# Kernel optimization log

Measured on AMD Instinct MI355X. Metric: run time of the kernel, lower is better.

Reference implementation:

```python
import jax, jax.numpy as jnp
from jax import lax
import numpy as np

K_F = 3                      # propagation kernel
NUM = K_F * K_F - 1          # 8 non-reference neighbors
IDX_REF = NUM // 2           # 4
PROP_TIME = 18
GAMMA = 0.5                  # affinity_gamma (TGASS)
EPS_AFF = 1e-8


def setup_inputs() -> dict:
    key = jax.random.key(0)
    k1, k2, k3, k4, k5 = jax.random.split(key, 5)
    B, H, W = 4, 352, 1216
    feat_init = jax.random.uniform(k1, (B, 1, H, W), jnp.float32) * 10.0   # initial depth
    guidance = jax.random.normal(k2, (B, NUM, H, W), jnp.float32)
    confidence = jax.random.uniform(k3, (B, 1, H, W), jnp.float32)
    # conv_offset_aff: Conv2d(ch_g=8 -> 3*num=24, k=3, pad=1). Zero-init in the
    # module is a training init; use small random weights for a meaningful test.
    w_oa = jax.random.normal(k4, (3 * NUM, NUM, 3, 3), jnp.float32) * 0.05
    b_oa = jax.random.normal(k5, (3 * NUM,), jnp.float32) * 0.01
    aff_scale = jnp.array([GAMMA * NUM], jnp.float32)  # TGASS learnable scale
    return {"feat_init": feat_init, "guidance": guidance, "confidence": confidence,
            "w_oa": w_oa, "b_oa": b_oa, "aff_scale": aff_scale}


def _offset_affinity(guidance, w_oa, b_oa, aff_scale):
    B, _, H, W = guidance.shape
    oa = lax.conv_general_dilated(guidance, w_oa, (1, 1), "SAME",
                                  dimension_numbers=("NCHW", "OIHW", "NCHW"))
    oa = oa + b_oa[None, :, None, None]
    o1, o2, aff = jnp.split(oa, 3, axis=1)            # each [B, 8, H, W]
    offset = jnp.concatenate([o1, o2], axis=1).reshape(B, NUM, 2, H, W)
    zeros_ref = jnp.zeros((B, 1, 2, H, W), offset.dtype)
    offset = jnp.concatenate([offset[:, :IDX_REF], zeros_ref, offset[:, IDX_REF:]],
                             axis=1).reshape(B, -1, H, W)  # [B, 2*9, H, W]
    # TGASS affinity
    aff = jnp.tanh(aff) / (aff_scale[0] + EPS_AFF)
    aff_abs_sum = jnp.sum(jnp.abs(aff), axis=1, keepdims=True) + 1e-4
    aff_abs_sum = jnp.maximum(aff_abs_sum, 1.0)       # TGASS clamp to >= 1
    aff = aff / aff_abs_sum
    aff_ref = 1.0 - jnp.sum(aff, axis=1, keepdims=True)
    aff = jnp.concatenate([aff[:, :IDX_REF], aff_ref, aff[:, IDX_REF:]], axis=1)
    return offset, aff                                 # [B,18,H,W], [B,9,H,W]


def _bilinear(f, ys, xs):
    # f: [H, W]; ys, xs: [K, H, W] float sample coords. Zero outside bounds (DCNv2).
    H, W = f.shape
    y0 = jnp.floor(ys); x0 = jnp.floor(xs)
    wy1 = ys - y0; wy0 = 1.0 - wy1
    wx1 = xs - x0; wx0 = 1.0 - wx1

    def g(yi, xi):
        valid = (yi >= 0) & (yi <= H - 1) & (xi >= 0) & (xi <= W - 1)
        yc = jnp.clip(yi, 0, H - 1).astype(jnp.int32)
        xc = jnp.clip(xi, 0, W - 1).astype(jnp.int32)
        return jnp.where(valid, f[yc, xc], 0.0)

    return (wy0 * wx0 * g(y0, x0) + wy0 * wx1 * g(y0, x0 + 1)
            + wy1 * wx0 * g(y0 + 1, x0) + wy1 * wx1 * g(y0 + 1, x0 + 1))


def _dcn(feat, offset, aff):
    # Modulated deformable conv with w=ones, b=0, stride=1, pad=1, groups=1.
    # feat [B,1,H,W], offset [B,2*9,H,W] ((dy,dx) pairs), aff [B,9,H,W] modulation.
    B, _, H, W = feat.shape
    KK = K_F * K_F
    off = offset.reshape(B, KK, 2, H, W)
    k = jnp.arange(KK)
    ky = (k // K_F - 1).astype(feat.dtype)            # kernel taps, pad=1
    kx = (k % K_F - 1).astype(feat.dtype)
    yg, xg = jnp.meshgrid(jnp.arange(H, dtype=feat.dtype),
                          jnp.arange(W, dtype=feat.dtype), indexing="ij")
    ys = yg[None, None] + ky[None, :, None, None] + off[:, :, 0]  # [B,9,H,W]
    xs = xg[None, None] + kx[None, :, None, None] + off[:, :, 1]
    sampled = jax.vmap(_bilinear)(feat[:, 0], ys, xs)             # [B,9,H,W]
    return jnp.sum(aff * sampled, axis=1, keepdims=True)          # [B,1,H,W]


def reference(feat_init, guidance, confidence, w_oa, b_oa, aff_scale):
    offset, aff = _offset_affinity(guidance, w_oa, b_oa, aff_scale)

    def step(feat, _):
        feat = _dcn(feat * confidence, offset, aff)
        return feat, None

    feat, _ = lax.scan(step, feat_init, None, length=PROP_TIME)
    return feat
```

## Files before the change

kernel.cpp:

```cpp
#include <hip/hip_runtime.h>

#define BB 4
#define HH 352
#define WW 1216
#define HW (HH * WW)
#define NPIX (BB * HW)
#define TX 4
#define CONV_THREADS 320

#define PAD_T 5
#define PAD_L 8
#define HP (HH + 2 * PAD_T)
#define WP (WW + 2 * PAD_L)
#define HWP (HP * WP)

#define TROWS 13
#define TCOLS 76
#define TSIZE (TROWS * TCOLS)


__global__ __launch_bounds__(CONV_THREADS) void conv_offsets_kernel(
    const float* __restrict__ guid, const float* __restrict__ w,
    const float* __restrict__ bias, unsigned* __restrict__ coordp)
{
    int tid = threadIdx.x;
    if (tid >= WW / TX) return;
    int bid = blockIdx.x;
    int row = (bid & 7) * 176 + (bid >> 3);
    int y = row % HH;
    int b = row / HH;
    int x0 = tid * TX;
    const float* gb = guid + (size_t)b * 8 * HW;

    float acc[16][TX];
#pragma unroll
    for (int o = 0; o < 16; ++o) {
        float bv = bias[o];
#pragma unroll
        for (int tx = 0; tx < TX; ++tx) acc[o][tx] = bv;
    }

#pragma unroll 1
    for (int c = 0; c < 8; ++c) {
        float g[3][6];
#pragma unroll
        for (int r = 0; r < 3; ++r) {
            int yy = y + r - 1;
            bool rv = (yy >= 0) && (yy < HH);
            const float* gr = gb + (size_t)c * HW + (size_t)yy * WW;
            if (rv) {
                const float4 m = *(const float4*)(gr + x0);
                g[r][1] = m.x; g[r][2] = m.y; g[r][3] = m.z; g[r][4] = m.w;
                g[r][0] = (x0 > 0) ? gr[x0 - 1] : 0.f;
                g[r][5] = (x0 + TX < WW) ? gr[x0 + TX] : 0.f;
            } else {
#pragma unroll
                for (int i = 0; i < 6; ++i) g[r][i] = 0.f;
            }
        }
#pragma unroll
        for (int r = 0; r < 3; ++r) {
#pragma unroll
            for (int i = 0; i < 3; ++i) {
                int tap = r * 3 + i;
#pragma unroll
                for (int o = 0; o < 16; ++o) {
                    float wv = w[o * 72 + c * 9 + tap];
#pragma unroll
                    for (int tx = 0; tx < TX; ++tx)
                        acc[o][tx] = fmaf(wv, g[r][i + tx], acc[o][tx]);
                }
            }
        }
    }

    int idx0 = row * WW + x0;
#pragma unroll
    for (int n = 0; n < 8; ++n) {
        int k = (n < 4) ? n : n + 1;
        float ky = (float)(k / 3 - 1), kx = (float)(k % 3 - 1);
        unsigned cw[TX];
#pragma unroll
        for (int tx = 0; tx < TX; ++tx) {
            float yr = ky + acc[2 * n][tx];
            float xr = kx + acc[2 * n + 1][tx];
            int yq = (int)lrintf((yr + 4.f) * 8192.f);
            int xq = (int)lrintf((xr + 4.f) * 8192.f);
            yq = min(max(yq, 0), 65535);
            xq = min(max(xq, 0), 65535);
            cw[tx] = (unsigned)yq | ((unsigned)xq << 16);
        }
        uint4 v = make_uint4(cw[0], cw[1], cw[2], cw[3]);
        *(uint4*)(coordp + (size_t)n * NPIX + idx0) = v;
    }
}

__global__ __launch_bounds__(CONV_THREADS) void conv_aff_kernel(
    const float* __restrict__ guid, const float* __restrict__ w,
    const float* __restrict__ bias, const float* __restrict__ scale_p,
    unsigned short* __restrict__ affp)
{
    int tid = threadIdx.x;
    if (tid >= WW / TX) return;
    int bid = blockIdx.x;
    int row = (bid & 7) * 176 + (bid >> 3);
    int y = row % HH;
    int b = row / HH;
    int x0 = tid * TX;
    const float* gb = guid + (size_t)b * 8 * HW;

    float acc[8][TX];
#pragma unroll
    for (int o = 0; o < 8; ++o) {
        float bv = bias[16 + o];
#pragma unroll
        for (int tx = 0; tx < TX; ++tx) acc[o][tx] = bv;
    }

#pragma unroll 1
    for (int c = 0; c < 8; ++c) {
        float g[3][6];
#pragma unroll
        for (int r = 0; r < 3; ++r) {
            int yy = y + r - 1;
            bool rv = (yy >= 0) && (yy < HH);
            const float* gr = gb + (size_t)c * HW + (size_t)yy * WW;
            if (rv) {
                const float4 m = *(const float4*)(gr + x0);
                g[r][1] = m.x; g[r][2] = m.y; g[r][3] = m.z; g[r][4] = m.w;
                g[r][0] = (x0 > 0) ? gr[x0 - 1] : 0.f;
                g[r][5] = (x0 + TX < WW) ? gr[x0 + TX] : 0.f;
            } else {
#pragma unroll
                for (int i = 0; i < 6; ++i) g[r][i] = 0.f;
            }
        }
#pragma unroll
        for (int r = 0; r < 3; ++r) {
#pragma unroll
            for (int i = 0; i < 3; ++i) {
                int tap = r * 3 + i;
#pragma unroll
                for (int o = 0; o < 8; ++o) {
                    float wv = w[(16 + o) * 72 + c * 9 + tap];
#pragma unroll
                    for (int tx = 0; tx < TX; ++tx)
                        acc[o][tx] = fmaf(wv, g[r][i + tx], acc[o][tx]);
                }
            }
        }
    }

    float sc = scale_p[0] + 1e-8f;
    unsigned short av[9][TX];

#pragma unroll
    for (int tx = 0; tx < TX; ++tx) {
        float a[8];
        float asum = 1e-4f;
#pragma unroll
        for (int n = 0; n < 8; ++n) {
            a[n] = tanhf(acc[n][tx]) / sc;
            asum += fabsf(a[n]);
        }
        asum = fmaxf(asum, 1.0f);
        float ssum = 0.f;
#pragma unroll
        for (int n = 0; n < 8; ++n) { a[n] = a[n] / asum; ssum += a[n]; }
        float aref = 1.0f - ssum;
#pragma unroll
        for (int k = 0; k < 9; ++k) {
            float aval = (k == 4) ? aref : a[(k < 4) ? k : k - 1];
            int q = (int)lrintf((aval + 1.f) * 20000.f);
            q = min(max(q, 0), 65535);
            av[k][tx] = (unsigned short)q;
        }
    }

    int idx0 = row * WW + x0;
#pragma unroll
    for (int k = 0; k < 9; ++k) {
        ushort4 v = make_ushort4(av[k][0], av[k][1], av[k][2], av[k][3]);
        *(ushort4*)(affp + (size_t)k * NPIX + idx0) = v;
    }
}

template <bool MULCONF>
__global__ __launch_bounds__(256) void prop_step_kernel(
    const float* __restrict__ fsrc, const unsigned short* __restrict__ affp,
    const unsigned* __restrict__ coordp, const float* __restrict__ conf,
    float* __restrict__ dst)
{
    __shared__ float tile[TSIZE];

    int bid = blockIdx.x;
    int xcd = bid & 7;
    int s = bid >> 3;
    int yband = xcd * 11 + s % 11;
    int rest = s / 11;
    int xb = rest % 19;
    int b = rest / 19;
    int t = threadIdx.x;
    int lx = t & 63, ly = t >> 6;
    int x = xb * 64 + lx;
    int y = yband * 4 + ly;
    int idx = (b * HH + y) * WW + x;

    unsigned cw[8];
#pragma unroll
    for (int n = 0; n < 8; ++n) cw[n] = coordp[(size_t)n * NPIX + idx];
    float ak[9];
#pragma unroll
    for (int k = 0; k < 9; ++k)
        ak[k] = fmaf((float)affp[(size_t)k * NPIX + idx], 5e-5f, -1.f);
    float cv = MULCONF ? conf[idx] : 0.f;

    {
        const float* gsrc = fsrc + (size_t)b * HWP
                          + (size_t)(yband * 4 + 1) * WP + (xb * 64 + 4);
        for (int i = t; i < TSIZE; i += 256)
            tile[i] = gsrc[(i / TCOLS) * WP + (i % TCOLS)];
    }
    __syncthreads();

    float fy = (float)ly;
    float fx = (float)lx;
    float res = ak[4] * tile[(ly + 4) * TCOLS + (lx + 4)];
#pragma unroll
    for (int n = 0; n < 8; ++n) {
        float ys = fmaf((float)(cw[n] & 0xffffu), 1.f / 8192.f, fy);
        float xs = fmaf((float)(cw[n] >> 16),     1.f / 8192.f, fx);
        float y0f = floorf(ys), x0f = floorf(xs);
        float wy1 = ys - y0f, wx1 = xs - x0f;
        float wy0 = 1.f - wy1, wx0 = 1.f - wx1;
        int o = (int)y0f * TCOLS + (int)x0f;
        float v00 = tile[o],         v01 = tile[o + 1];
        float v10 = tile[o + TCOLS], v11 = tile[o + TCOLS + 1];
        float sv = wy0 * (wx0 * v00 + wx1 * v01) + wy1 * (wx0 * v10 + wx1 * v11);
        int k = (n < 4) ? n : n + 1;
        res = fmaf(ak[k], sv, res);
    }
    if (MULCONF) {
        res *= cv;
        dst[(size_t)b * HWP + (y + PAD_T) * WP + (x + PAD_L)] = res;
    } else {
        dst[idx] = res;
    }
}

__global__ __launch_bounds__(256) void zero_kernel(float4* __restrict__ p, int n4)
{
    int i = blockIdx.x * blockDim.x + threadIdx.x;
    if (i < n4) p[i] = make_float4(0.f, 0.f, 0.f, 0.f);
}

__global__ __launch_bounds__(256) void mulpad_kernel(
    const float* __restrict__ a, const float* __restrict__ c, float* __restrict__ o)
{
    int t = threadIdx.x;
    int x = blockIdx.x * 64 + (t & 63);
    int y = blockIdx.y * 4 + (t >> 6);
    int b = blockIdx.z;
    int idx = (b * HH + y) * WW + x;
    o[(size_t)b * HWP + (y + PAD_T) * WP + (x + PAD_L)] = a[idx] * c[idx];
}

extern "C" void kernel_launch(void* const* d_in, const int* in_sizes, int n_in,
                              void* d_out, int out_size, void* d_ws, size_t ws_size,
                              hipStream_t stream)
{
    const float* feat_init  = (const float*)d_in[0];
    const float* guidance   = (const float*)d_in[1];
    const float* confidence = (const float*)d_in[2];
    const float* w_oa       = (const float*)d_in[3];
    const float* b_oa       = (const float*)d_in[4];
    const float* aff_scale  = (const float*)d_in[5];
    float* out = (float*)d_out;

    const size_t N = (size_t)NPIX;
    unsigned short* affp = (unsigned short*)d_ws;
    unsigned* coordp = (unsigned*)(affp + 9 * N);
    float* fc0 = (float*)(coordp + 8 * N);
    float* fc1 = fc0 + (size_t)BB * HWP;

    const dim3 mgrid(WW / 64, HH / 4, BB);
    const int n4 = 2 * BB * HWP / 4;
    zero_kernel<<<(n4 + 255) / 256, 256, 0, stream>>>((float4*)fc0, n4);
    mulpad_kernel<<<mgrid, 256, 0, stream>>>(feat_init, confidence, fc0);
    conv_offsets_kernel<<<BB * HH, CONV_THREADS, 0, stream>>>(
        guidance, w_oa, b_oa, coordp);
    conv_aff_kernel<<<BB * HH, CONV_THREADS, 0, stream>>>(
        guidance, w_oa, b_oa, aff_scale, affp);

    const int pblocks = (WW / 64) * (HH / 4) * BB;
    float* bufs[2] = {fc0, fc1};
    const int T = 18;
    for (int i = 0; i < T; ++i) {
        const float* src = bufs[i & 1];
        if (i < T - 1) {
            float* dst = bufs[(i + 1) & 1];
            prop_step_kernel<true><<<pblocks, 256, 0, stream>>>(
                src, affp, coordp, confidence, dst);
        } else {
            prop_step_kernel<false><<<pblocks, 256, 0, stream>>>(
                src, affp, coordp, confidence, out);
        }
    }
}
```

Baseline: 589.1 us.

## Interleave per-pixel coords and affinities into one 64-byte record table

Replaces the planar coordinate (8 planes) and affinity (9 planes) arrays with an array-of-structs table holding 16 words per pixel, so each propagation step loads three uint4s plus one word per pixel instead of 17 strided scalar loads. The conv kernels now handle 2 pixels per thread with 640 threads and write the record layout. The record is padded to 64 bytes, so per-step traffic rises slightly (about 64 bytes against 50), in exchange for fewer, wider, contiguous load instructions.

```diff
diff --git a/kernel.cpp b/kernel.cpp
--- a/kernel.cpp
+++ b/kernel.cpp
@@ -5,8 +5,6 @@
 #define WW 1216
 #define HW (HH * WW)
 #define NPIX (BB * HW)
-#define TX 4
-#define CONV_THREADS 320
 
 #define PAD_T 5
 #define PAD_L 8
@@ -19,43 +17,46 @@
 #define TSIZE (TROWS * TCOLS)
 
 
-__global__ __launch_bounds__(CONV_THREADS) void conv_offsets_kernel(
+#define OTX 2
+#define OTHREADS 640
+
+__global__ __launch_bounds__(OTHREADS) void conv_offsets_kernel(
     const float* __restrict__ guid, const float* __restrict__ w,
-    const float* __restrict__ bias, unsigned* __restrict__ coordp)
+    const float* __restrict__ bias, unsigned* __restrict__ tab)
 {
     int tid = threadIdx.x;
-    if (tid >= WW / TX) return;
+    if (tid >= WW / OTX) return;
     int bid = blockIdx.x;
     int row = (bid & 7) * 176 + (bid >> 3);
     int y = row % HH;
     int b = row / HH;
-    int x0 = tid * TX;
+    int x0 = tid * OTX;
     const float* gb = guid + (size_t)b * 8 * HW;
 
-    float acc[16][TX];
+    float acc[16][OTX];
 #pragma unroll
     for (int o = 0; o < 16; ++o) {
         float bv = bias[o];
 #pragma unroll
-        for (int tx = 0; tx < TX; ++tx) acc[o][tx] = bv;
+        for (int tx = 0; tx < OTX; ++tx) acc[o][tx] = bv;
     }
 
 #pragma unroll 1
     for (int c = 0; c < 8; ++c) {
-        float g[3][6];
+        float g[3][4];
 #pragma unroll
         for (int r = 0; r < 3; ++r) {
             int yy = y + r - 1;
             bool rv = (yy >= 0) && (yy < HH);
             const float* gr = gb + (size_t)c * HW + (size_t)yy * WW;
             if (rv) {
-                const float4 m = *(const float4*)(gr + x0);
-                g[r][1] = m.x; g[r][2] = m.y; g[r][3] = m.z; g[r][4] = m.w;
+                const float2 m = *(const float2*)(gr + x0);
+                g[r][1] = m.x; g[r][2] = m.y;
                 g[r][0] = (x0 > 0) ? gr[x0 - 1] : 0.f;
-                g[r][5] = (x0 + TX < WW) ? gr[x0 + TX] : 0.f;
+                g[r][3] = (x0 + OTX < WW) ? gr[x0 + OTX] : 0.f;
             } else {
 #pragma unroll
-                for (int i = 0; i < 6; ++i) g[r][i] = 0.f;
+                for (int i = 0; i < 4; ++i) g[r][i] = 0.f;
             }
         }
 #pragma unroll
@@ -67,7 +68,7 @@
                 for (int o = 0; o < 16; ++o) {
                     float wv = w[o * 72 + c * 9 + tap];
 #pragma unroll
-                    for (int tx = 0; tx < TX; ++tx)
+                    for (int tx = 0; tx < OTX; ++tx)
                         acc[o][tx] = fmaf(wv, g[r][i + tx], acc[o][tx]);
                 }
             }
@@ -76,63 +77,64 @@
 
     int idx0 = row * WW + x0;
 #pragma unroll
-    for (int n = 0; n < 8; ++n) {
-        int k = (n < 4) ? n : n + 1;
-        float ky = (float)(k / 3 - 1), kx = (float)(k % 3 - 1);
-        unsigned cw[TX];
-#pragma unroll
-        for (int tx = 0; tx < TX; ++tx) {
+    for (int tx = 0; tx < OTX; ++tx) {
+        unsigned cw[8];
+#pragma unroll
+        for (int n = 0; n < 8; ++n) {
+            int k = (n < 4) ? n : n + 1;
+            float ky = (float)(k / 3 - 1), kx = (float)(k % 3 - 1);
             float yr = ky + acc[2 * n][tx];
             float xr = kx + acc[2 * n + 1][tx];
             int yq = (int)lrintf((yr + 4.f) * 8192.f);
             int xq = (int)lrintf((xr + 4.f) * 8192.f);
             yq = min(max(yq, 0), 65535);
             xq = min(max(xq, 0), 65535);
-            cw[tx] = (unsigned)yq | ((unsigned)xq << 16);
-        }
-        uint4 v = make_uint4(cw[0], cw[1], cw[2], cw[3]);
-        *(uint4*)(coordp + (size_t)n * NPIX + idx0) = v;
-    }
-}
-
-__global__ __launch_bounds__(CONV_THREADS) void conv_aff_kernel(
+            cw[n] = (unsigned)yq | ((unsigned)xq << 16);
+        }
+        unsigned* rec = tab + (size_t)(idx0 + tx) * 16;
+        *(uint4*)(rec)     = make_uint4(cw[0], cw[1], cw[2], cw[3]);
+        *(uint4*)(rec + 4) = make_uint4(cw[4], cw[5], cw[6], cw[7]);
+    }
+}
+
+__global__ __launch_bounds__(OTHREADS) void conv_aff_kernel(
     const float* __restrict__ guid, const float* __restrict__ w,
     const float* __restrict__ bias, const float* __restrict__ scale_p,
-    unsigned short* __restrict__ affp)
+    unsigned* __restrict__ tab)
 {
     int tid = threadIdx.x;
-    if (tid >= WW / TX) return;
+    if (tid >= WW / OTX) return;
     int bid = blockIdx.x;
     int row = (bid & 7) * 176 + (bid >> 3);
     int y = row % HH;
     int b = row / HH;
-    int x0 = tid * TX;
+    int x0 = tid * OTX;
     const float* gb = guid + (size_t)b * 8 * HW;
 
-    float acc[8][TX];
+    float acc[8][OTX];
 #pragma unroll
     for (int o = 0; o < 8; ++o) {
         float bv = bias[16 + o];
 #pragma unroll
-        for (int tx = 0; tx < TX; ++tx) acc[o][tx] = bv;
+        for (int tx = 0; tx < OTX; ++tx) acc[o][tx] = bv;
     }
 
 #pragma unroll 1
     for (int c = 0; c < 8; ++c) {
-        float g[3][6];
+        float g[3][4];
 #pragma unroll
         for (int r = 0; r < 3; ++r) {
             int yy = y + r - 1;
             bool rv = (yy >= 0) && (yy < HH);
             const float* gr = gb + (size_t)c * HW + (size_t)yy * WW;
             if (rv) {
-                const float4 m = *(const float4*)(gr + x0);
-                g[r][1] = m.x; g[r][2] = m.y; g[r][3] = m.z; g[r][4] = m.w;
+                const float2 m = *(const float2*)(gr + x0);
+                g[r][1] = m.x; g[r][2] = m.y;
                 g[r][0] = (x0 > 0) ? gr[x0 - 1] : 0.f;
-                g[r][5] = (x0 + TX < WW) ? gr[x0 + TX] : 0.f;
+                g[r][3] = (x0 + OTX < WW) ? gr[x0 + OTX] : 0.f;
             } else {
 #pragma unroll
-                for (int i = 0; i < 6; ++i) g[r][i] = 0.f;
+                for (int i = 0; i < 4; ++i) g[r][i] = 0.f;
             }
         }
 #pragma unroll
@@ -144,7 +146,7 @@
                 for (int o = 0; o < 8; ++o) {
                     float wv = w[(16 + o) * 72 + c * 9 + tap];
 #pragma unroll
-                    for (int tx = 0; tx < TX; ++tx)
+                    for (int tx = 0; tx < OTX; ++tx)
                         acc[o][tx] = fmaf(wv, g[r][i + tx], acc[o][tx]);
                 }
             }
@@ -152,10 +154,10 @@
     }
 
     float sc = scale_p[0] + 1e-8f;
-    unsigned short av[9][TX];
-
-#pragma unroll
-    for (int tx = 0; tx < TX; ++tx) {
+    int idx0 = row * WW + x0;
+
+#pragma unroll
+    for (int tx = 0; tx < OTX; ++tx) {
         float a[8];
         float asum = 1e-4f;
 #pragma unroll
@@ -168,28 +170,27 @@
 #pragma unroll
         for (int n = 0; n < 8; ++n) { a[n] = a[n] / asum; ssum += a[n]; }
         float aref = 1.0f - ssum;
+
+        unsigned av[9];
 #pragma unroll
         for (int k = 0; k < 9; ++k) {
             float aval = (k == 4) ? aref : a[(k < 4) ? k : k - 1];
             int q = (int)lrintf((aval + 1.f) * 20000.f);
-            q = min(max(q, 0), 65535);
-            av[k][tx] = (unsigned short)q;
-        }
-    }
-
-    int idx0 = row * WW + x0;
-#pragma unroll
-    for (int k = 0; k < 9; ++k) {
-        ushort4 v = make_ushort4(av[k][0], av[k][1], av[k][2], av[k][3]);
-        *(ushort4*)(affp + (size_t)k * NPIX + idx0) = v;
+            av[k] = (unsigned)min(max(q, 0), 65535);
+        }
+        unsigned* rec = tab + (size_t)(idx0 + tx) * 16;
+        *(uint4*)(rec + 8) = make_uint4(av[0] | (av[1] << 16),
+                                        av[2] | (av[3] << 16),
+                                        av[4] | (av[5] << 16),
+                                        av[6] | (av[7] << 16));
+        rec[12] = av[8];
     }
 }
 
 template <bool MULCONF>
 __global__ __launch_bounds__(256) void prop_step_kernel(
-    const float* __restrict__ fsrc, const unsigned short* __restrict__ affp,
-    const unsigned* __restrict__ coordp, const float* __restrict__ conf,
-    float* __restrict__ dst)
+    const float* __restrict__ fsrc, const unsigned* __restrict__ tab,
+    const float* __restrict__ conf, float* __restrict__ dst)
 {
     __shared__ float tile[TSIZE];
 
@@ -206,13 +207,11 @@
     int y = yband * 4 + ly;
     int idx = (b * HH + y) * WW + x;
 
-    unsigned cw[8];
-#pragma unroll
-    for (int n = 0; n < 8; ++n) cw[n] = coordp[(size_t)n * NPIX + idx];
-    float ak[9];
-#pragma unroll
-    for (int k = 0; k < 9; ++k)
-        ak[k] = fmaf((float)affp[(size_t)k * NPIX + idx], 5e-5f, -1.f);
+    const uint4* rp = (const uint4*)(tab + (size_t)idx * 16);
+    uint4 c0 = rp[0];
+    uint4 c1 = rp[1];
+    uint4 au = rp[2];
+    unsigned a8 = tab[(size_t)idx * 16 + 12];
     float cv = MULCONF ? conf[idx] : 0.f;
 
     {
@@ -223,13 +222,22 @@
     }
     __syncthreads();
 
+    unsigned cwv[8] = {c0.x, c0.y, c0.z, c0.w, c1.x, c1.y, c1.z, c1.w};
+    unsigned akU[9] = {au.x & 0xffffu, au.x >> 16, au.y & 0xffffu, au.y >> 16,
+                       au.z & 0xffffu, au.z >> 16, au.w & 0xffffu, au.w >> 16,
+                       a8 & 0xffffu};
+
     float fy = (float)ly;
     float fx = (float)lx;
-    float res = ak[4] * tile[(ly + 4) * TCOLS + (lx + 4)];
+    float a4 = fmaf((float)akU[4], 5e-5f, -1.f);
+    float res = a4 * tile[(ly + 4) * TCOLS + (lx + 4)];
 #pragma unroll
     for (int n = 0; n < 8; ++n) {
-        float ys = fmaf((float)(cw[n] & 0xffffu), 1.f / 8192.f, fy);
-        float xs = fmaf((float)(cw[n] >> 16),     1.f / 8192.f, fx);
+        int k = (n < 4) ? n : n + 1;
+        float ak = fmaf((float)akU[k], 5e-5f, -1.f);
+        unsigned q = cwv[n];
+        float ys = fmaf((float)(q & 0xffffu), 1.f / 8192.f, fy);
+        float xs = fmaf((float)(q >> 16),     1.f / 8192.f, fx);
         float y0f = floorf(ys), x0f = floorf(xs);
         float wy1 = ys - y0f, wx1 = xs - x0f;
         float wy0 = 1.f - wy1, wx0 = 1.f - wx1;
@@ -237,8 +245,7 @@
         float v00 = tile[o],         v01 = tile[o + 1];
         float v10 = tile[o + TCOLS], v11 = tile[o + TCOLS + 1];
         float sv = wy0 * (wx0 * v00 + wx1 * v01) + wy1 * (wx0 * v10 + wx1 * v11);
-        int k = (n < 4) ? n : n + 1;
-        res = fmaf(ak[k], sv, res);
+        res = fmaf(ak, sv, res);
     }
     if (MULCONF) {
         res *= cv;
@@ -278,19 +285,18 @@
     float* out = (float*)d_out;
 
     const size_t N = (size_t)NPIX;
-    unsigned short* affp = (unsigned short*)d_ws;
-    unsigned* coordp = (unsigned*)(affp + 9 * N);
-    float* fc0 = (float*)(coordp + 8 * N);
+    unsigned* tab = (unsigned*)d_ws;
+    float* fc0 = (float*)(tab + 16 * N);
     float* fc1 = fc0 + (size_t)BB * HWP;
 
     const dim3 mgrid(WW / 64, HH / 4, BB);
     const int n4 = 2 * BB * HWP / 4;
     zero_kernel<<<(n4 + 255) / 256, 256, 0, stream>>>((float4*)fc0, n4);
     mulpad_kernel<<<mgrid, 256, 0, stream>>>(feat_init, confidence, fc0);
-    conv_offsets_kernel<<<BB * HH, CONV_THREADS, 0, stream>>>(
-        guidance, w_oa, b_oa, coordp);
-    conv_aff_kernel<<<BB * HH, CONV_THREADS, 0, stream>>>(
-        guidance, w_oa, b_oa, aff_scale, affp);
+    conv_offsets_kernel<<<BB * HH, OTHREADS, 0, stream>>>(
+        guidance, w_oa, b_oa, tab);
+    conv_aff_kernel<<<BB * HH, OTHREADS, 0, stream>>>(
+        guidance, w_oa, b_oa, aff_scale, tab);
 
     const int pblocks = (WW / 64) * (HH / 4) * BB;
     float* bufs[2] = {fc0, fc1};
@@ -300,10 +306,10 @@
         if (i < T - 1) {
             float* dst = bufs[(i + 1) & 1];
             prop_step_kernel<true><<<pblocks, 256, 0, stream>>>(
-                src, affp, coordp, confidence, dst);
+                src, tab, confidence, dst);
         } else {
             prop_step_kernel<false><<<pblocks, 256, 0, stream>>>(
-                src, affp, coordp, confidence, out);
-        }
-    }
-}
+                src, tab, confidence, out);
+        }
+    }
+}
```

Result: slower. 649.1 us (+10.2%).

## Fuse offset and affinity convolutions into one shared-memory tiled kernel

Applied to the files above, without the earlier changes.

Replaces the two separate row-based convolution kernels (offsets and affinity) with a single kernel that computes all 24 output channels per pixel. Guidance data for a 64x4 tile plus halo is staged in shared memory, so each input is read once instead of twice from global memory and neighbouring rows are reused. Each thread now handles one pixel instead of four, which gives up register reuse of weights across pixels and narrows stores to scalar writes. The convolution is a small part of the total time next to the 18 propagation steps.

```diff
diff --git a/kernel.cpp b/kernel.cpp
--- a/kernel.cpp
+++ b/kernel.cpp
@@ -5,8 +5,6 @@
 #define WW 1216
 #define HW (HH * WW)
 #define NPIX (BB * HW)
-#define TX 4
-#define CONV_THREADS 320
 
 #define PAD_T 5
 #define PAD_L 8
@@ -18,170 +16,92 @@
 #define TCOLS 76
 #define TSIZE (TROWS * TCOLS)
 
-
-__global__ __launch_bounds__(CONV_THREADS) void conv_offsets_kernel(
+#define GT_W 66
+#define GT_CH 396
+#define GT_SIZE (8 * GT_CH)
+
+
+__global__ __launch_bounds__(256) void conv_fused_kernel(
     const float* __restrict__ guid, const float* __restrict__ w,
-    const float* __restrict__ bias, unsigned* __restrict__ coordp)
-{
-    int tid = threadIdx.x;
-    if (tid >= WW / TX) return;
-    int bid = blockIdx.x;
-    int row = (bid & 7) * 176 + (bid >> 3);
-    int y = row % HH;
-    int b = row / HH;
-    int x0 = tid * TX;
-    const float* gb = guid + (size_t)b * 8 * HW;
-
-    float acc[16][TX];
-#pragma unroll
-    for (int o = 0; o < 16; ++o) {
-        float bv = bias[o];
-#pragma unroll
-        for (int tx = 0; tx < TX; ++tx) acc[o][tx] = bv;
-    }
+    const float* __restrict__ bias, const float* __restrict__ scale_p,
+    unsigned short* __restrict__ affp, unsigned* __restrict__ coordp)
+{
+    __shared__ float gt[GT_SIZE];
+
+    int bx = blockIdx.x, by = blockIdx.y, b = blockIdx.z;
+    int t = threadIdx.x;
+    int lx = t & 63, ly = t >> 6;
+    int x = bx * 64 + lx;
+    int y = by * 4 + ly;
+
+    {
+        const float* gb = guid + (size_t)b * 8 * HW;
+        int gy0 = by * 4 - 1, gx0 = bx * 64 - 1;
+        for (int i = t; i < GT_SIZE; i += 256) {
+            int c = i / GT_CH, rem = i - c * GT_CH;
+            int r = rem / GT_W, col = rem - r * GT_W;
+            int gy = gy0 + r, gx = gx0 + col;
+            float v = 0.f;
+            if (gy >= 0 && gy < HH && gx >= 0 && gx < WW)
+                v = gb[(size_t)c * HW + gy * WW + gx];
+            gt[i] = v;
+        }
+    }
+    __syncthreads();
+
+    float acc[24];
+#pragma unroll
+    for (int o = 0; o < 24; ++o) acc[o] = bias[o];
 
 #pragma unroll 1
     for (int c = 0; c < 8; ++c) {
-        float g[3][6];
-#pragma unroll
-        for (int r = 0; r < 3; ++r) {
-            int yy = y + r - 1;
-            bool rv = (yy >= 0) && (yy < HH);
-            const float* gr = gb + (size_t)c * HW + (size_t)yy * WW;
-            if (rv) {
-                const float4 m = *(const float4*)(gr + x0);
-                g[r][1] = m.x; g[r][2] = m.y; g[r][3] = m.z; g[r][4] = m.w;
-                g[r][0] = (x0 > 0) ? gr[x0 - 1] : 0.f;
-                g[r][5] = (x0 + TX < WW) ? gr[x0 + TX] : 0.f;
-            } else {
-#pragma unroll
-                for (int i = 0; i < 6; ++i) g[r][i] = 0.f;
-            }
+        float v[9];
+#pragma unroll
+        for (int r = 0; r < 3; ++r)
+#pragma unroll
+            for (int i = 0; i < 3; ++i)
+                v[r * 3 + i] = gt[c * GT_CH + (ly + r) * GT_W + lx + i];
+#pragma unroll
+        for (int tap = 0; tap < 9; ++tap) {
+#pragma unroll
+            for (int o = 0; o < 24; ++o)
+                acc[o] = fmaf(w[o * 72 + c * 9 + tap], v[tap], acc[o]);
         }
-#pragma unroll
-        for (int r = 0; r < 3; ++r) {
-#pragma unroll
-            for (int i = 0; i < 3; ++i) {
-                int tap = r * 3 + i;
-#pragma unroll
-                for (int o = 0; o < 16; ++o) {
-                    float wv = w[o * 72 + c * 9 + tap];
-#pragma unroll
-                    for (int tx = 0; tx < TX; ++tx)
-                        acc[o][tx] = fmaf(wv, g[r][i + tx], acc[o][tx]);
-                }
-            }
-        }
-    }
-
-    int idx0 = row * WW + x0;
+    }
+
+    float sc = scale_p[0] + 1e-8f;
+    float a[8];
+    float asum = 1e-4f;
+#pragma unroll
+    for (int n = 0; n < 8; ++n) {
+        a[n] = tanhf(acc[16 + n]) / sc;
+        asum += fabsf(a[n]);
+    }
+    asum = fmaxf(asum, 1.0f);
+    float ssum = 0.f;
+#pragma unroll
+    for (int n = 0; n < 8; ++n) { a[n] = a[n] / asum; ssum += a[n]; }
+    float aref = 1.0f - ssum;
+
+    int idx = (b * HH + y) * WW + x;
 #pragma unroll
     for (int n = 0; n < 8; ++n) {
         int k = (n < 4) ? n : n + 1;
         float ky = (float)(k / 3 - 1), kx = (float)(k % 3 - 1);
-        unsigned cw[TX];
-#pragma unroll
-        for (int tx = 0; tx < TX; ++tx) {
-            float yr = ky + acc[2 * n][tx];
-            float xr = kx + acc[2 * n + 1][tx];
-            int yq = (int)lrintf((yr + 4.f) * 8192.f);
-            int xq = (int)lrintf((xr + 4.f) * 8192.f);
-            yq = min(max(yq, 0), 65535);
-            xq = min(max(xq, 0), 65535);
-            cw[tx] = (unsigned)yq | ((unsigned)xq << 16);
-        }
-        uint4 v = make_uint4(cw[0], cw[1], cw[2], cw[3]);
-        *(uint4*)(coordp + (size_t)n * NPIX + idx0) = v;
-    }
-}
-
-__global__ __launch_bounds__(CONV_THREADS) void conv_aff_kernel(
-    const float* __restrict__ guid, const float* __restrict__ w,
-    const float* __restrict__ bias, const float* __restrict__ scale_p,
-    unsigned short* __restrict__ affp)
-{
-    int tid = threadIdx.x;
-    if (tid >= WW / TX) return;
-    int bid = blockIdx.x;
-    int row = (bid & 7) * 176 + (bid >> 3);
-    int y = row % HH;
-    int b = row / HH;
-    int x0 = tid * TX;
-    const float* gb = guid + (size_t)b * 8 * HW;
-
-    float acc[8][TX];
-#pragma unroll
-    for (int o = 0; o < 8; ++o) {
-        float bv = bias[16 + o];
-#pragma unroll
-        for (int tx = 0; tx < TX; ++tx) acc[o][tx] = bv;
-    }
-
-#pragma unroll 1
-    for (int c = 0; c < 8; ++c) {
-        float g[3][6];
-#pragma unroll
-        for (int r = 0; r < 3; ++r) {
-            int yy = y + r - 1;
-            bool rv = (yy >= 0) && (yy < HH);
-            const float* gr = gb + (size_t)c * HW + (size_t)yy * WW;
-            if (rv) {
-                const float4 m = *(const float4*)(gr + x0);
-                g[r][1] = m.x; g[r][2] = m.y; g[r][3] = m.z; g[r][4] = m.w;
-                g[r][0] = (x0 > 0) ? gr[x0 - 1] : 0.f;
-                g[r][5] = (x0 + TX < WW) ? gr[x0 + TX] : 0.f;
-            } else {
-#pragma unroll
-                for (int i = 0; i < 6; ++i) g[r][i] = 0.f;
-            }
-        }
-#pragma unroll
-        for (int r = 0; r < 3; ++r) {
-#pragma unroll
-            for (int i = 0; i < 3; ++i) {
-                int tap = r * 3 + i;
-#pragma unroll
-                for (int o = 0; o < 8; ++o) {
-                    float wv = w[(16 + o) * 72 + c * 9 + tap];
-#pragma unroll
-                    for (int tx = 0; tx < TX; ++tx)
-                        acc[o][tx] = fmaf(wv, g[r][i + tx], acc[o][tx]);
-                }
-            }
-        }
-    }
-
-    float sc = scale_p[0] + 1e-8f;
-    unsigned short av[9][TX];
-
-#pragma unroll
-    for (int tx = 0; tx < TX; ++tx) {
-        float a[8];
-        float asum = 1e-4f;
-#pragma unroll
-        for (int n = 0; n < 8; ++n) {
-            a[n] = tanhf(acc[n][tx]) / sc;
-            asum += fabsf(a[n]);
-        }
-        asum = fmaxf(asum, 1.0f);
-        float ssum = 0.f;
-#pragma unroll
-        for (int n = 0; n < 8; ++n) { a[n] = a[n] / asum; ssum += a[n]; }
-        float aref = 1.0f - ssum;
-#pragma unroll
-        for (int k = 0; k < 9; ++k) {
-            float aval = (k == 4) ? aref : a[(k < 4) ? k : k - 1];
-            int q = (int)lrintf((aval + 1.f) * 20000.f);
-            q = min(max(q, 0), 65535);
-            av[k][tx] = (unsigned short)q;
-        }
-    }
-
-    int idx0 = row * WW + x0;
+        float yr = ky + acc[2 * n];
+        float xr = kx + acc[2 * n + 1];
+        int yq = (int)lrintf((yr + 4.f) * 8192.f);
+        int xq = (int)lrintf((xr + 4.f) * 8192.f);
+        yq = min(max(yq, 0), 65535);
+        xq = min(max(xq, 0), 65535);
+        coordp[(size_t)n * NPIX + idx] = (unsigned)yq | ((unsigned)xq << 16);
+    }
 #pragma unroll
     for (int k = 0; k < 9; ++k) {
-        ushort4 v = make_ushort4(av[k][0], av[k][1], av[k][2], av[k][3]);
-        *(ushort4*)(affp + (size_t)k * NPIX + idx0) = v;
+        float aval = (k == 4) ? aref : a[(k < 4) ? k : k - 1];
+        int q = (int)lrintf((aval + 1.f) * 20000.f);
+        q = min(max(q, 0), 65535);
+        affp[(size_t)k * NPIX + idx] = (unsigned short)q;
     }
 }
 
@@ -287,10 +207,8 @@
     const int n4 = 2 * BB * HWP / 4;
     zero_kernel<<<(n4 + 255) / 256, 256, 0, stream>>>((float4*)fc0, n4);
     mulpad_kernel<<<mgrid, 256, 0, stream>>>(feat_init, confidence, fc0);
-    conv_offsets_kernel<<<BB * HH, CONV_THREADS, 0, stream>>>(
-        guidance, w_oa, b_oa, coordp);
-    conv_aff_kernel<<<BB * HH, CONV_THREADS, 0, stream>>>(
-        guidance, w_oa, b_oa, aff_scale, affp);
+    conv_fused_kernel<<<mgrid, 256, 0, stream>>>(
+        guidance, w_oa, b_oa, aff_scale, affp, coordp);
 
     const int pblocks = (WW / 64) * (HH / 4) * BB;
     float* bufs[2] = {fc0, fc1};
```

Result: slower. 629.5 us (+6.9%).
